# Performance work log

Measured on AMD Instinct MI355X. Metric: run time of the kernel, lower is better.

## Reference

```python
import jax, jax.numpy as jnp
import numpy as np

B, N, DIN, DOUT, H = 4, 2048, 256, 256, 4
HD = DOUT // H
NEG_SLOPE = 0.2


def setup_inputs() -> dict:
    key = jax.random.key(0)
    k1, k2, k3, k4, k5 = jax.random.split(key, 5)
    x = jax.random.normal(k1, (B, N, DIN), dtype=jnp.float32)
    adj = jax.random.randint(k2, (B, N, N), 0, 2).astype(jnp.float32)
    # ensure self-loops so every softmax row has at least one valid entry
    adj = jnp.maximum(adj, jnp.eye(N, dtype=jnp.float32)[None])
    # xavier-uniform-ish scales
    w_bound = float(np.sqrt(6.0 / (DIN + DOUT)))
    a_bound = float(np.sqrt(6.0 / (1 + HD)))
    W = jax.random.uniform(k3, (DOUT, DIN), jnp.float32, -w_bound, w_bound)
    a_src = jax.random.uniform(k4, (H, HD), jnp.float32, -a_bound, a_bound)
    a_dst = jax.random.uniform(k5, (H, HD), jnp.float32, -a_bound, a_bound)
    return {"x": x, "adj": adj, "W": W, "a_src": a_src, "a_dst": a_dst}


def reference(x, adj, W, a_src, a_dst):
    b, n, _ = x.shape
    h = (x @ W.T).reshape(b, n, H, HD)                      # [B,N,H,HD]
    s_src = jnp.einsum('bnhd,hd->bnh', h, a_src)            # [B,N,H]
    s_dst = jnp.einsum('bnhd,hd->bnh', h, a_dst)            # [B,N,H]
    # e[b,i,j,h] = leaky_relu(s_src[b,i,h] + s_dst[b,j,h])
    e = jax.nn.leaky_relu(s_src[:, :, None, :] + s_dst[:, None, :, :], NEG_SLOPE)
    e = jnp.where(adj[..., None] == 0, -jnp.inf, e)         # [B,N,N,H]
    alpha = jax.nn.softmax(e, axis=2)                       # softmax over j (dropout is identity at eval)
    out = jnp.einsum('bijh,bjhd->bihd', alpha, h)           # weighted aggregate
    return out.reshape(b, n, DOUT)
```

## Files before the change

### kernel.cpp

```cpp
#include <hip/hip_runtime.h>
#include <math.h>

#define Bb   4
#define Nn   2048
#define Dd   256
#define Hh   4
#define HDd  64
#define BN   (Bb * Nn)

typedef float v4f __attribute__((ext_vector_type(4)));
typedef short v8s __attribute__((ext_vector_type(8)));

__device__ __forceinline__ unsigned rne_bf16(float f) {
    unsigned u = __float_as_uint(f);
    u += 0x7fffu + ((u >> 16) & 1u);
    return u >> 16;
}

__global__ __launch_bounds__(256, 2) void k_gemm(const float* __restrict__ x,
                                                 const float* __restrict__ W,
                                                 const float* __restrict__ a_src,
                                                 const float* __restrict__ a_dst,
                                                 unsigned short* __restrict__ hbf,
                                                 float* __restrict__ ssrc,
                                                 float* __restrict__ sdst) {
    __shared__ __align__(16) unsigned short xs[2][64 * 72];
    __shared__ __align__(16) unsigned short wsm[2][64 * 72];
    __shared__ float asd[128];

    const int tid = threadIdx.x;
    const int m0 = (int)(blockIdx.x >> 2) * 64;
    const int head = (int)blockIdx.x & 3;
    const int n0 = head * 64;
    const int b = m0 >> 11;
    const int i0loc = m0 & 2047;

    if (tid < 128) {
        int sel = tid >> 6, d = tid & 63;
        asd[tid] = sel ? a_dst[n0 + d] : a_src[n0 + d];
    }

    const int wv = tid >> 6, ln = tid & 63, l15 = ln & 15, l4 = ln >> 4;
    const int mh = wv >> 1, nh = wv & 1;
    const int srow = tid >> 2, kq = (tid & 3) * 16;

    v4f acc[2][2];
#pragma unroll
    for (int g = 0; g < 2; ++g)
#pragma unroll
        for (int t = 0; t < 2; ++t) acc[g][t] = (v4f){0.f, 0.f, 0.f, 0.f};

    for (int st = 0; st < 4; ++st) {
        const int k0 = st * 64;
        __syncthreads();
        {
            float xf[16], wf[16];
            const float* xp = x + (size_t)(m0 + srow) * Dd + k0 + kq;
            const float* wp = W + (size_t)(n0 + srow) * Dd + k0 + kq;
#pragma unroll
            for (int q = 0; q < 4; ++q) {
                *(float4*)&xf[q * 4] = *(const float4*)(xp + q * 4);
                *(float4*)&wf[q * 4] = *(const float4*)(wp + q * 4);
            }
            unsigned xh[8], xl[8], wh[8], wl[8];
#pragma unroll
            for (int j = 0; j < 8; ++j) {
                unsigned h0 = rne_bf16(xf[2 * j]), h1 = rne_bf16(xf[2 * j + 1]);
                float l0 = xf[2 * j] - __uint_as_float(h0 << 16);
                float l1 = xf[2 * j + 1] - __uint_as_float(h1 << 16);
                xh[j] = h0 | (h1 << 16);
                xl[j] = rne_bf16(l0) | (rne_bf16(l1) << 16);
                unsigned g0 = rne_bf16(wf[2 * j]), g1 = rne_bf16(wf[2 * j + 1]);
                float m0f = wf[2 * j] - __uint_as_float(g0 << 16);
                float m1f = wf[2 * j + 1] - __uint_as_float(g1 << 16);
                wh[j] = g0 | (g1 << 16);
                wl[j] = rne_bf16(m0f) | (rne_bf16(m1f) << 16);
            }
            *(uint4*)(xs[0] + srow * 72 + kq)     = make_uint4(xh[0], xh[1], xh[2], xh[3]);
            *(uint4*)(xs[0] + srow * 72 + kq + 8) = make_uint4(xh[4], xh[5], xh[6], xh[7]);
            *(uint4*)(xs[1] + srow * 72 + kq)     = make_uint4(xl[0], xl[1], xl[2], xl[3]);
            *(uint4*)(xs[1] + srow * 72 + kq + 8) = make_uint4(xl[4], xl[5], xl[6], xl[7]);
            *(uint4*)(wsm[0] + srow * 72 + kq)     = make_uint4(wh[0], wh[1], wh[2], wh[3]);
            *(uint4*)(wsm[0] + srow * 72 + kq + 8) = make_uint4(wh[4], wh[5], wh[6], wh[7]);
            *(uint4*)(wsm[1] + srow * 72 + kq)     = make_uint4(wl[0], wl[1], wl[2], wl[3]);
            *(uint4*)(wsm[1] + srow * 72 + kq + 8) = make_uint4(wl[4], wl[5], wl[6], wl[7]);
        }
        __syncthreads();
        {
            v8s ah[2][2], al[2][2], bh_[2][2], bl_[2][2];
#pragma unroll
            for (int g = 0; g < 2; ++g)
#pragma unroll
                for (int kh = 0; kh < 2; ++kh) {
                    int ro = (mh * 32 + g * 16 + l15) * 72 + kh * 32 + l4 * 8;
                    ah[g][kh] = *(const v8s*)(xs[0] + ro);
                    al[g][kh] = *(const v8s*)(xs[1] + ro);
                }
#pragma unroll
            for (int t = 0; t < 2; ++t)
#pragma unroll
                for (int kh = 0; kh < 2; ++kh) {
                    int ro = (nh * 32 + t * 16 + l15) * 72 + kh * 32 + l4 * 8;
                    bh_[t][kh] = *(const v8s*)(wsm[0] + ro);
                    bl_[t][kh] = *(const v8s*)(wsm[1] + ro);
                }
#pragma unroll
            for (int g = 0; g < 2; ++g)
#pragma unroll
                for (int t = 0; t < 2; ++t)
#pragma unroll
                    for (int kh = 0; kh < 2; ++kh) {
                        acc[g][t] = __builtin_amdgcn_mfma_f32_16x16x32_bf16(ah[g][kh], bh_[t][kh], acc[g][t], 0, 0, 0);
                        acc[g][t] = __builtin_amdgcn_mfma_f32_16x16x32_bf16(al[g][kh], bh_[t][kh], acc[g][t], 0, 0, 0);
                        acc[g][t] = __builtin_amdgcn_mfma_f32_16x16x32_bf16(ah[g][kh], bl_[t][kh], acc[g][t], 0, 0, 0);
                    }
        }
    }

    __syncthreads();
    float* T = (float*)&xs[0][0];
#pragma unroll
    for (int g = 0; g < 2; ++g)
#pragma unroll
        for (int t = 0; t < 2; ++t)
#pragma unroll
            for (int r = 0; r < 4; ++r) {
                int d = nh * 32 + t * 16 + l15;
                int m = mh * 32 + g * 16 + l4 * 4 + r;
                T[d * 67 + m] = acc[g][t][r];
            }
    __syncthreads();
    if (tid < 128) {
        int m = tid & 63, sel = tid >> 6;
        float s = 0.f;
#pragma unroll
        for (int d = 0; d < 64; ++d) s += T[d * 67 + m] * asd[sel * 64 + d];
        (sel ? sdst : ssrc)[(size_t)head * BN + (size_t)b * Nn + i0loc + m] = s;
        int dloc = tid >> 1, jh = tid & 1;
        const float* row = T + dloc * 67 + jh * 32;
        unsigned pk[16];
#pragma unroll
        for (int jj = 0; jj < 16; ++jj)
            pk[jj] = rne_bf16(row[jj * 2]) | (rne_bf16(row[jj * 2 + 1]) << 16);
        unsigned short* dst = hbf +
            ((size_t)((b * 64 + (i0loc >> 5) + jh) * 256 + head * HDd + dloc)) * 32;
        uint4* d4 = (uint4*)dst;
        d4[0] = make_uint4(pk[0], pk[1], pk[2], pk[3]);
        d4[1] = make_uint4(pk[4], pk[5], pk[6], pk[7]);
        d4[2] = make_uint4(pk[8], pk[9], pk[10], pk[11]);
        d4[3] = make_uint4(pk[12], pk[13], pk[14], pk[15]);
    }
}

__global__ __launch_bounds__(512, 4) void k_aggr(const unsigned short* __restrict__ hbf,
                                                 const float* __restrict__ adj,
                                                 const float* __restrict__ ssrc,
                                                 const float* __restrict__ sdst,
                                                 float* __restrict__ out) {
    __shared__ __align__(16) float sdl[4 * 2048];
    __shared__ __align__(16) float red[4 * 64 * 20];

    const int tid = threadIdx.x;
    const int bid = (int)blockIdx.x;
    const int b  = bid >> 7;
    const int i0 = (bid & 127) * 16;

    const int wv = tid >> 6;
    const int h  = wv & 3;
    const int jh = wv >> 2;
    const int ln = tid & 63, l15 = ln & 15, l4 = ln >> 4;

    for (int q = tid; q < 2048; q += 512) {
        int hh = q >> 9, j = (q & 511) * 4;
        *(float4*)&sdl[hh * 2048 + j] =
            *(const float4*)(sdst + (size_t)hh * BN + (size_t)b * Nn + j);
    }

    const int irow = i0 + l15;
    const float ss = ssrc[(size_t)h * BN + (size_t)b * Nn + irow];
    const float* adjr = adj + ((size_t)b * Nn + irow) * Nn + jh * 1024 + l4 * 8;
    const unsigned short* hb0 = hbf +
        ((size_t)b * 64 * 256 + (size_t)(h * HDd + l15)) * 32 + l4 * 8;
    const float* sdb = sdl + h * 2048 + jh * 1024 + l4 * 8;

    const v8s ones = {0x3F80, 0x3F80, 0x3F80, 0x3F80, 0x3F80, 0x3F80, 0x3F80, 0x3F80};

    v4f acc0 = (v4f){0.f, 0.f, 0.f, 0.f}, acc1 = acc0, acc2 = acc0, acc3 = acc0, zac = acc0;
    v8s bb0, bb1, bb2, bb3, bb4, bb5, bb6, bb7;
    float4 ajA0, ajA1, ajA2, ajA3, ajB0, ajB1, ajB2, ajB3;

    __syncthreads();

#define LOADB(S_) do {                                                        \
        const unsigned short* hq_ = hb0 + (size_t)(jh * 16 + (S_)) * 16384;   \
        bb0 = *(const v8s*)(hq_ + 0);                                         \
        bb1 = *(const v8s*)(hq_ + 8192);                                      \
        bb2 = *(const v8s*)(hq_ + 512);                                       \
        bb3 = *(const v8s*)(hq_ + 8192 + 512);                                \
        bb4 = *(const v8s*)(hq_ + 1024);                                      \
        bb5 = *(const v8s*)(hq_ + 8192 + 1024);                               \
        bb6 = *(const v8s*)(hq_ + 1536);                                      \
        bb7 = *(const v8s*)(hq_ + 8192 + 1536);                               \
    } while (0)

#define LOADADJ(S_, A0_, A1_, A2_, A3_) do {                                  \
        const float* ap_ = adjr + ((S_) & 15) * 64;                           \
        A0_ = *(const float4*)(ap_);                                          \
        A1_ = *(const float4*)(ap_ + 4);                                      \
        A2_ = *(const float4*)(ap_ + 32);                                     \
        A3_ = *(const float4*)(ap_ + 36);                                     \
    } while (0)

#define GENW(ssv, sdv, ajv) ({                                                \
        float e_ = (ssv) + (sdv);                                             \
        e_ = fmaxf(e_, 0.2f * e_);                                            \
        (ajv) * __expf(e_);                                                   \
    })

#define GENFRAG(dst, ajx, ajy, sdx, sdy) do {                                 \
        float w0_ = GENW(ss, sdx.x, ajx.x);                                   \
        float w1_ = GENW(ss, sdx.y, ajx.y);                                   \
        float w2_ = GENW(ss, sdx.z, ajx.z);                                   \
        float w3_ = GENW(ss, sdx.w, ajx.w);                                   \
        float w4_ = GENW(ss, sdy.x, ajy.x);                                   \
        float w5_ = GENW(ss, sdy.y, ajy.y);                                   \
        float w6_ = GENW(ss, sdy.z, ajy.z);                                   \
        float w7_ = GENW(ss, sdy.w, ajy.w);                                   \
        union { v8s v; unsigned u[4]; } P_;                                   \
        P_.u[0] = rne_bf16(w0_) | (rne_bf16(w1_) << 16);                      \
        P_.u[1] = rne_bf16(w2_) | (rne_bf16(w3_) << 16);                      \
        P_.u[2] = rne_bf16(w4_) | (rne_bf16(w5_) << 16);                      \
        P_.u[3] = rne_bf16(w6_) | (rne_bf16(w7_) << 16);                      \
        dst = P_.v;                                                           \
    } while (0)

#define STEPX(S_, A0_, A1_, A2_, A3_) do {                                    \
        const float* sdp_ = sdb + (S_) * 64;                                  \
        const float4 sd0_ = *(const float4*)(sdp_);                           \
        const float4 sd1_ = *(const float4*)(sdp_ + 4);                       \
        const float4 sd2_ = *(const float4*)(sdp_ + 32);                      \
        const float4 sd3_ = *(const float4*)(sdp_ + 36);                      \
        v8s afr0_, afr1_;                                                     \
        GENFRAG(afr0_, A0_, A1_, sd0_, sd1_);                                 \
        GENFRAG(afr1_, A2_, A3_, sd2_, sd3_);                                 \
        acc0 = __builtin_amdgcn_mfma_f32_16x16x32_bf16(afr0_, bb0, acc0, 0, 0, 0); \
        acc1 = __builtin_amdgcn_mfma_f32_16x16x32_bf16(afr0_, bb2, acc1, 0, 0, 0); \
        acc2 = __builtin_amdgcn_mfma_f32_16x16x32_bf16(afr0_, bb4, acc2, 0, 0, 0); \
        acc3 = __builtin_amdgcn_mfma_f32_16x16x32_bf16(afr0_, bb6, acc3, 0, 0, 0); \
        zac  = __builtin_amdgcn_mfma_f32_16x16x32_bf16(afr0_, ones, zac, 0, 0, 0); \
        acc0 = __builtin_amdgcn_mfma_f32_16x16x32_bf16(afr1_, bb1, acc0, 0, 0, 0); \
        acc1 = __builtin_amdgcn_mfma_f32_16x16x32_bf16(afr1_, bb3, acc1, 0, 0, 0); \
        acc2 = __builtin_amdgcn_mfma_f32_16x16x32_bf16(afr1_, bb5, acc2, 0, 0, 0); \
        acc3 = __builtin_amdgcn_mfma_f32_16x16x32_bf16(afr1_, bb7, acc3, 0, 0, 0); \
        zac  = __builtin_amdgcn_mfma_f32_16x16x32_bf16(afr1_, ones, zac, 0, 0, 0); \
    } while (0)

    LOADADJ(0, ajA0, ajA1, ajA2, ajA3);
#pragma unroll 1
    for (int s = 0; s < 16; s += 2) {
        LOADB(s);
        LOADADJ(s + 1, ajB0, ajB1, ajB2, ajB3);
        __builtin_amdgcn_sched_barrier(0);
        STEPX(s, ajA0, ajA1, ajA2, ajA3);
        LOADB(s + 1);
        LOADADJ(s + 2, ajA0, ajA1, ajA2, ajA3);
        __builtin_amdgcn_sched_barrier(0);
        STEPX(s + 1, ajB0, ajB1, ajB2, ajB3);
    }

#undef LOADB
#undef LOADADJ
#undef GENW
#undef GENFRAG
#undef STEPX

    float* rp = red + (h * 64 + ln) * 20;
    if (jh) {
        *(v4f*)(rp + 0)  = acc0;
        *(v4f*)(rp + 4)  = acc1;
        *(v4f*)(rp + 8)  = acc2;
        *(v4f*)(rp + 12) = acc3;
        *(v4f*)(rp + 16) = zac;
    }
    __syncthreads();
    if (!jh) {
        acc0 += *(const v4f*)(rp + 0);
        acc1 += *(const v4f*)(rp + 4);
        acc2 += *(const v4f*)(rp + 8);
        acc3 += *(const v4f*)(rp + 12);
        zac  += *(const v4f*)(rp + 16);
        float zi[4];
#pragma unroll
        for (int r = 0; r < 4; ++r) zi[r] = 1.f / zac[r];
        float* op = out + ((size_t)b * Nn + i0 + l4 * 4) * Dd + h * HDd + l15;
#pragma unroll
        for (int r = 0; r < 4; ++r) {
            op[(size_t)r * Dd + 0]  = acc0[r] * zi[r];
            op[(size_t)r * Dd + 16] = acc1[r] * zi[r];
            op[(size_t)r * Dd + 32] = acc2[r] * zi[r];
            op[(size_t)r * Dd + 48] = acc3[r] * zi[r];
        }
    }
}

extern "C" void kernel_launch(void* const* d_in, const int* in_sizes, int n_in,
                              void* d_out, int out_size, void* d_ws, size_t ws_size,
                              hipStream_t stream) {
    const float* x     = (const float*)d_in[0];
    const float* adj   = (const float*)d_in[1];
    const float* W     = (const float*)d_in[2];
    const float* a_src = (const float*)d_in[3];
    const float* a_dst = (const float*)d_in[4];
    float* out = (float*)d_out;

    unsigned short* hbf = (unsigned short*)d_ws;
    float* ssrc = (float*)(hbf + (size_t)Bb * Nn * Dd);
    float* sdst = ssrc + (size_t)Hh * BN;

    k_gemm<<<dim3(512), dim3(256), 0, stream>>>(x, W, a_src, a_dst, hbf, ssrc, sdst);
    k_aggr<<<dim3(512), dim3(512), 0, stream>>>(hbf, adj, ssrc, sdst, out);
}
```

Measured before the change: 168.1 us.

## Pack adjacency into bitmask in extra gemm blocks, read bits in aggregation

Result: faster. 154.6 us (-8.0%).

```diff
diff --git a/kernel.cpp b/kernel.cpp
--- a/kernel.cpp
+++ b/kernel.cpp
@@ -21,12 +21,37 @@
                                                  const float* __restrict__ W,
                                                  const float* __restrict__ a_src,
                                                  const float* __restrict__ a_dst,
+                                                 const float* __restrict__ adj,
                                                  unsigned short* __restrict__ hbf,
                                                  float* __restrict__ ssrc,
-                                                 float* __restrict__ sdst) {
+                                                 float* __restrict__ sdst,
+                                                 unsigned long long* __restrict__ bitadj) {
     __shared__ __align__(16) unsigned short xs[2][64 * 72];
     __shared__ __align__(16) unsigned short wsm[2][64 * 72];
     __shared__ float asd[128];
+
+    if (blockIdx.x >= 512) {
+        const int gw = ((int)blockIdx.x - 512) * 4 + ((int)threadIdx.x >> 6);
+        const int lane = (int)threadIdx.x & 63;
+#pragma unroll 1
+        for (int w = gw * 4; w < 262144; w += 8192 * 4) {
+            float v0 = adj[(size_t)((w + 0) >> 5) * 2048 + ((w + 0) & 31) * 64 + lane];
+            float v1 = adj[(size_t)((w + 1) >> 5) * 2048 + ((w + 1) & 31) * 64 + lane];
+            float v2 = adj[(size_t)((w + 2) >> 5) * 2048 + ((w + 2) & 31) * 64 + lane];
+            float v3 = adj[(size_t)((w + 3) >> 5) * 2048 + ((w + 3) & 31) * 64 + lane];
+            unsigned long long m0 = __ballot(v0 != 0.0f);
+            unsigned long long m1 = __ballot(v1 != 0.0f);
+            unsigned long long m2 = __ballot(v2 != 0.0f);
+            unsigned long long m3 = __ballot(v3 != 0.0f);
+            if (lane == 0) {
+                bitadj[w + 0] = m0;
+                bitadj[w + 1] = m1;
+                bitadj[w + 2] = m2;
+                bitadj[w + 3] = m3;
+            }
+        }
+        return;
+    }
 
     const int tid = threadIdx.x;
     const int m0 = (int)(blockIdx.x >> 2) * 64;
@@ -153,7 +178,7 @@
 }
 
 __global__ __launch_bounds__(512, 4) void k_aggr(const unsigned short* __restrict__ hbf,
-                                                 const float* __restrict__ adj,
+                                                 const unsigned long long* __restrict__ bitadj,
                                                  const float* __restrict__ ssrc,
                                                  const float* __restrict__ sdst,
                                                  float* __restrict__ out) {
@@ -178,16 +203,18 @@
 
     const int irow = i0 + l15;
     const float ss = ssrc[(size_t)h * BN + (size_t)b * Nn + irow];
-    const float* adjr = adj + ((size_t)b * Nn + irow) * Nn + jh * 1024 + l4 * 8;
+    const unsigned char* ajr = (const unsigned char*)bitadj +
+        ((size_t)b * Nn + irow) * 256 + jh * 128;
     const unsigned short* hb0 = hbf +
         ((size_t)b * 64 * 256 + (size_t)(h * HDd + l15)) * 32 + l4 * 8;
     const float* sdb = sdl + h * 2048 + jh * 1024 + l4 * 8;
+    const unsigned mbase = 1u << (l4 * 8);
 
     const v8s ones = {0x3F80, 0x3F80, 0x3F80, 0x3F80, 0x3F80, 0x3F80, 0x3F80, 0x3F80};
 
     v4f acc0 = (v4f){0.f, 0.f, 0.f, 0.f}, acc1 = acc0, acc2 = acc0, acc3 = acc0, zac = acc0;
     v8s bb0, bb1, bb2, bb3, bb4, bb5, bb6, bb7;
-    float4 ajA0, ajA1, ajA2, ajA3, ajB0, ajB1, ajB2, ajB3;
+    uint2 ajA, ajB;
 
     __syncthreads();
 
@@ -203,29 +230,27 @@
         bb7 = *(const v8s*)(hq_ + 8192 + 1536);                               \
     } while (0)
 
-#define LOADADJ(S_, A0_, A1_, A2_, A3_) do {                                  \
-        const float* ap_ = adjr + ((S_) & 15) * 64;                           \
-        A0_ = *(const float4*)(ap_);                                          \
-        A1_ = *(const float4*)(ap_ + 4);                                      \
-        A2_ = *(const float4*)(ap_ + 32);                                     \
-        A3_ = *(const float4*)(ap_ + 36);                                     \
+#define LOADADJ(S_, A_) do {                                                  \
+        A_ = *(const uint2*)(ajr + ((S_) & 15) * 8);                          \
     } while (0)
 
-#define GENW(ssv, sdv, ajv) ({                                                \
-        float e_ = (ssv) + (sdv);                                             \
+#define GENP(sdv) ({                                                          \
+        float e_ = ss + (sdv);                                                \
         e_ = fmaxf(e_, 0.2f * e_);                                            \
-        (ajv) * __expf(e_);                                                   \
+        __expf(e_);                                                           \
     })
 
-#define GENFRAG(dst, ajx, ajy, sdx, sdy) do {                                 \
-        float w0_ = GENW(ss, sdx.x, ajx.x);                                   \
-        float w1_ = GENW(ss, sdx.y, ajx.y);                                   \
-        float w2_ = GENW(ss, sdx.z, ajx.z);                                   \
-        float w3_ = GENW(ss, sdx.w, ajx.w);                                   \
-        float w4_ = GENW(ss, sdy.x, ajy.x);                                   \
-        float w5_ = GENW(ss, sdy.y, ajy.y);                                   \
-        float w6_ = GENW(ss, sdy.z, ajy.z);                                   \
-        float w7_ = GENW(ss, sdy.w, ajy.w);                                   \
+#define SEL(W_, K_, P_) (((W_) & (mbase << (K_))) ? (P_) : 0.0f)
+
+#define GENFRAG(dst, W_, sdx, sdy) do {                                       \
+        float p0_ = GENP(sdx.x), p1_ = GENP(sdx.y);                           \
+        float p2_ = GENP(sdx.z), p3_ = GENP(sdx.w);                           \
+        float p4_ = GENP(sdy.x), p5_ = GENP(sdy.y);                           \
+        float p6_ = GENP(sdy.z), p7_ = GENP(sdy.w);                           \
+        float w0_ = SEL(W_, 0, p0_), w1_ = SEL(W_, 1, p1_);                   \
+        float w2_ = SEL(W_, 2, p2_), w3_ = SEL(W_, 3, p3_);                   \
+        float w4_ = SEL(W_, 4, p4_), w5_ = SEL(W_, 5, p5_);                   \
+        float w6_ = SEL(W_, 6, p6_), w7_ = SEL(W_, 7, p7_);                   \
         union { v8s v; unsigned u[4]; } P_;                                   \
         P_.u[0] = rne_bf16(w0_) | (rne_bf16(w1_) << 16);                      \
         P_.u[1] = rne_bf16(w2_) | (rne_bf16(w3_) << 16);                      \
@@ -234,15 +259,15 @@
         dst = P_.v;                                                           \
     } while (0)
 
-#define STEPX(S_, A0_, A1_, A2_, A3_) do {                                    \
+#define STEPX(S_, AJ_) do {                                                   \
         const float* sdp_ = sdb + (S_) * 64;                                  \
         const float4 sd0_ = *(const float4*)(sdp_);                           \
         const float4 sd1_ = *(const float4*)(sdp_ + 4);                       \
         const float4 sd2_ = *(const float4*)(sdp_ + 32);                      \
         const float4 sd3_ = *(const float4*)(sdp_ + 36);                      \
         v8s afr0_, afr1_;                                                     \
-        GENFRAG(afr0_, A0_, A1_, sd0_, sd1_);                                 \
-        GENFRAG(afr1_, A2_, A3_, sd2_, sd3_);                                 \
+        GENFRAG(afr0_, AJ_.x, sd0_, sd1_);                                    \
+        GENFRAG(afr1_, AJ_.y, sd2_, sd3_);                                    \
         acc0 = __builtin_amdgcn_mfma_f32_16x16x32_bf16(afr0_, bb0, acc0, 0, 0, 0); \
         acc1 = __builtin_amdgcn_mfma_f32_16x16x32_bf16(afr0_, bb2, acc1, 0, 0, 0); \
         acc2 = __builtin_amdgcn_mfma_f32_16x16x32_bf16(afr0_, bb4, acc2, 0, 0, 0); \
@@ -255,22 +280,23 @@
         zac  = __builtin_amdgcn_mfma_f32_16x16x32_bf16(afr1_, ones, zac, 0, 0, 0); \
     } while (0)
 
-    LOADADJ(0, ajA0, ajA1, ajA2, ajA3);
+    LOADADJ(0, ajA);
 #pragma unroll 1
     for (int s = 0; s < 16; s += 2) {
         LOADB(s);
-        LOADADJ(s + 1, ajB0, ajB1, ajB2, ajB3);
+        LOADADJ(s + 1, ajB);
         __builtin_amdgcn_sched_barrier(0);
-        STEPX(s, ajA0, ajA1, ajA2, ajA3);
+        STEPX(s, ajA);
         LOADB(s + 1);
-        LOADADJ(s + 2, ajA0, ajA1, ajA2, ajA3);
+        LOADADJ(s + 2, ajA);
         __builtin_amdgcn_sched_barrier(0);
-        STEPX(s + 1, ajB0, ajB1, ajB2, ajB3);
+        STEPX(s + 1, ajB);
     }
 
 #undef LOADB
 #undef LOADADJ
-#undef GENW
+#undef GENP
+#undef SEL
 #undef GENFRAG
 #undef STEPX
 
@@ -316,7 +342,9 @@
     unsigned short* hbf = (unsigned short*)d_ws;
     float* ssrc = (float*)(hbf + (size_t)Bb * Nn * Dd);
     float* sdst = ssrc + (size_t)Hh * BN;
-
-    k_gemm<<<dim3(512), dim3(256), 0, stream>>>(x, W, a_src, a_dst, hbf, ssrc, sdst);
-    k_aggr<<<dim3(512), dim3(512), 0, stream>>>(hbf, adj, ssrc, sdst, out);
+    unsigned long long* bitadj = (unsigned long long*)(sdst + (size_t)Hh * BN);
+
+    k_gemm<<<dim3(2560), dim3(256), 0, stream>>>(x, W, a_src, a_dst, adj,
+                                                 hbf, ssrc, sdst, bitadj);
+    k_aggr<<<dim3(512), dim3(512), 0, stream>>>(hbf, bitadj, ssrc, sdst, out);
 }
```
